# Performance work log

Measured on AMD Instinct MI355X. Metric: run time of the kernel, lower is better.

Reference implementation:

```python
import jax, jax.numpy as jnp
import numpy as np
from math import sqrt


def setup_inputs() -> dict:
    key = jax.random.key(0)
    ks = jax.random.split(key, 10)
    N, C = 192, 96  # C = N // 2
    n, h, w = 8, 64, 64
    s = lambda fan_in: 1.0 / np.sqrt(fan_in)
    return {
        "x": jax.random.normal(ks[0], (n, N, h, w), dtype=jnp.float32),
        "pe": jax.random.normal(ks[1], (N, 120, 120), dtype=jnp.float32) * 0.02,
        "wq": jax.random.normal(ks[2], (C, N), dtype=jnp.float32) * s(N),
        "bq": jax.random.normal(ks[3], (C,), dtype=jnp.float32) * 0.01,
        "wk": jax.random.normal(ks[4], (C, N), dtype=jnp.float32) * s(N),
        "bk": jax.random.normal(ks[5], (C,), dtype=jnp.float32) * 0.01,
        "wv": jax.random.normal(ks[6], (C, N), dtype=jnp.float32) * s(N),
        "bv": jax.random.normal(ks[7], (C,), dtype=jnp.float32) * 0.01,
        "wz": jax.random.normal(ks[8], (N, C), dtype=jnp.float32) * s(C),
        "bz": jax.random.normal(ks[9], (N,), dtype=jnp.float32) * 0.01,
    }


def _conv1x1(x, w, b):
    # x: [n, cin, h, w]; w: [cout, cin]; b: [cout]
    return jnp.einsum("oc,nchw->nohw", w, x) + b[None, :, None, None]


def reference(x, pe, wq, bq, wk, bk, wv, bv, wz, bz):
    n, c_in, h, w = x.shape
    hw = h * w
    # 2D positional encoding, sliced to the actual spatial size
    x = x + pe[None, :, :h, :w]
    c = wq.shape[0]  # N // 2
    q = _conv1x1(x, wq, bq).reshape(n, c, hw)   # [n, c, hw]
    k = _conv1x1(x, wk, bk).reshape(n, c, hw)   # [n, c, hw]
    v = _conv1x1(x, wv, bv).reshape(n, c, hw)   # [n, c, hw]
    scale = sqrt(hw)
    # logits[n, i, j] = sum_c q[n,c,i] * k[n,c,j]
    logits = jnp.einsum("nci,ncj->nij", q, k) / scale  # [n, hw, hw]
    weights = jax.nn.softmax(logits, axis=-1)
    # z[n, c, i] = sum_j weights[n,i,j] * v[n,c,j]
    z = jnp.einsum("nij,ncj->nci", weights, v).reshape(n, c, h, w)
    z = _conv1x1(z, wz, bz)  # [n, N, h, w]
    return x + z
```

## Files before the change

### kernel.cpp

```cpp
#include <hip/hip_runtime.h>
#include <hip/hip_bf16.h>

#define HW 4096
#define CIN 192
#define CMID 96

typedef __attribute__((ext_vector_type(8))) short bf16x8;
typedef __attribute__((ext_vector_type(4))) float f32x4;
typedef __attribute__((ext_vector_type(16))) float f32x16;
typedef __attribute__((ext_vector_type(4))) unsigned int u32x4;

static __device__ __forceinline__ unsigned short f2bf(float f) {
    union { float f; unsigned int u; } v;
    v.f = f;
    unsigned int r = v.u + 0x7fffu + ((v.u >> 16) & 1u);
    return (unsigned short)(r >> 16);
}
static __device__ __forceinline__ float b2f(unsigned short h) {
    union { unsigned int u; float f; } v;
    v.u = ((unsigned int)h) << 16;
    return v.f;
}

static __device__ __forceinline__ void gload16(const void* g, void* l) {
    __builtin_amdgcn_global_load_lds(
        (const __attribute__((address_space(1))) unsigned int*)g,
        (__attribute__((address_space(3))) unsigned int*)l, 16, 0, 0);
}

#define SCQ (0.015625f * 1.44269504089f)

__global__ __launch_bounds__(256) void convw_kernel(
    const float* __restrict__ wq, const float* __restrict__ wk,
    const float* __restrict__ wv, const float* __restrict__ wz,
    unsigned short* __restrict__ wqkvb, unsigned short* __restrict__ wzb)
{
    int idx = blockIdx.x * 256 + threadIdx.x;
    if (idx < 3 * CMID * CIN) {
        int m = idx / (CMID * CIN), r = idx % (CMID * CIN);
        const float* w = (m == 0) ? wq : ((m == 1) ? wk : wv);
        wqkvb[idx] = f2bf(w[r]);
    } else if (idx < 3 * CMID * CIN + CIN * CMID) {
        int r = idx - 3 * CMID * CIN;
        wzb[r] = f2bf(wz[r]);
    }
}

__global__ __launch_bounds__(256) void qkv_kernel(
    const float* __restrict__ x, const float* __restrict__ pe,
    const unsigned short* __restrict__ wqkvb,
    const float* __restrict__ bq, const float* __restrict__ bk,
    const float* __restrict__ bv,
    unsigned short* __restrict__ Q, unsigned short* __restrict__ K,
    unsigned short* __restrict__ V)
{
    const int n = blockIdx.y, i0 = blockIdx.x * 64, t = threadIdx.x;
    __shared__ unsigned short xt[64 * 200];

    for (int idx = t; idx < CIN * 64; idx += 256) {
        int c = idx >> 6, il = idx & 63;
        float v = x[((size_t)n * CIN + c) * HW + i0 + il]
                + pe[c * 14400 + blockIdx.x * 120 + il];
        xt[il * 200 + c] = f2bf(v);
    }
    __syncthreads();

    const int w = t >> 6, lane = t & 63, l15 = lane & 15, lg = lane >> 4;
    const int p0 = w * 16;

    bf16x8 af[6];
    #pragma unroll
    for (int f = 0; f < 6; ++f)
        af[f] = *(const bf16x8*)(xt + (p0 + l15) * 200 + f * 32 + lg * 8);

    #pragma unroll
    for (int ct = 0; ct < 18; ++ct) {
        const int m = ct / 6, c6 = ct % 6;
        f32x4 acc = (f32x4){0.f, 0.f, 0.f, 0.f};
        const unsigned short* wrow = wqkvb + (ct * 16 + l15) * CIN + lg * 8;
        #pragma unroll
        for (int f = 0; f < 6; ++f) {
            bf16x8 wf = *(const bf16x8*)(wrow + f * 32);
            if (m < 2)
                acc = __builtin_amdgcn_mfma_f32_16x16x32_bf16(wf, af[f], acc, 0, 0, 0);
            else
                acc = __builtin_amdgcn_mfma_f32_16x16x32_bf16(af[f], wf, acc, 0, 0, 0);
        }
        if (m < 2) {
            f32x4 bv4 = *(const f32x4*)(((m == 0) ? bq : bk) + c6 * 16 + lg * 4);
            ushort4 pk4;
            if (m == 0) {
                pk4.x = f2bf((acc[0] + bv4[0]) * SCQ);
                pk4.y = f2bf((acc[1] + bv4[1]) * SCQ);
                pk4.z = f2bf((acc[2] + bv4[2]) * SCQ);
                pk4.w = f2bf((acc[3] + bv4[3]) * SCQ);
            } else {
                pk4.x = f2bf(acc[0] + bv4[0]);
                pk4.y = f2bf(acc[1] + bv4[1]);
                pk4.z = f2bf(acc[2] + bv4[2]);
                pk4.w = f2bf(acc[3] + bv4[3]);
            }
            unsigned short* dst = ((m == 0) ? Q : K) + (size_t)n * HW * CMID;
            *(ushort4*)(dst + (size_t)(i0 + p0 + l15) * CMID + c6 * 16 + lg * 4) = pk4;
        } else {
            const float bias = bv[c6 * 16 + l15];
            ushort4 pk4;
            pk4.x = f2bf(acc[0] + bias); pk4.y = f2bf(acc[1] + bias);
            pk4.z = f2bf(acc[2] + bias); pk4.w = f2bf(acc[3] + bias);
            *(ushort4*)(V + (size_t)n * CMID * HW + (size_t)(c6 * 16 + l15) * HW
                          + i0 + p0 + lg * 4) = pk4;
        }
    }
}

__global__ __launch_bounds__(256, 4) void attn_kernel(
    const unsigned short* __restrict__ Q, const unsigned short* __restrict__ K,
    const unsigned short* __restrict__ V,
    unsigned short* __restrict__ zp, float* __restrict__ lp)
{
    const int bid = blockIdx.x;
    const int n  = bid & 7;
    const int jh = bid >> 8;
    const int bx = (bid >> 3) & 31;

    const int t = threadIdx.x, w = t >> 6, lane = t & 63;
    const int l31 = lane & 31, hi = lane >> 5;
    const int ib = bx * 128 + w * 32;

    __shared__ unsigned short Ks[2][32 * 128];
    __shared__ unsigned short Vs[2][96 * 64];

    const unsigned short* Qb = Q + (size_t)n * HW * CMID;
    const unsigned short* Kb = K + (size_t)n * HW * CMID;
    const unsigned short* Vb = V + (size_t)n * CMID * HW;

    bf16x8 qf[6];
    #pragma unroll
    for (int kc = 0; kc < 6; ++kc)
        qf[kc] = *(const bf16x8*)(Qb + (size_t)(ib + l31) * CMID + kc * 16 + hi * 8);

    int ksoff[2], vsoff[3];
    #pragma unroll
    for (int s = 0; s < 2; ++s) {
        int row = 4 * (w * 2 + s) + (lane >> 4);
        ksoff[s] = row * CMID + (((lane & 15) ^ (row & 7)) * 8);
    }
    #pragma unroll
    for (int s = 0; s < 3; ++s) {
        int c = 8 * (w * 3 + s) + (lane >> 3);
        vsoff[s] = c * HW + (((lane & 7) ^ (c & 7)) * 8);
    }

#define STAGE_K(J0, BUF) do {                                                      \
    _Pragma("unroll") for (int s = 0; s < 2; ++s)                                  \
        gload16(Kb + (size_t)(J0) * CMID + ksoff[s], &Ks[BUF][(w * 2 + s) * 512]); \
} while (0)
#define STAGE_V(J0, BUF) do {                                                      \
    _Pragma("unroll") for (int s = 0; s < 3; ++s)                                  \
        gload16(Vb + (size_t)(J0) + vsoff[s], &Vs[BUF][(w * 3 + s) * 512]);        \
} while (0)

    const int j00 = jh * 1024;
    STAGE_K(j00, 0);
    STAGE_V(j00, 0);

    f32x16 O[3];
    #pragma unroll
    for (int e = 0; e < 16; ++e) { O[0][e] = 0.f; O[1][e] = 0.f; O[2][e] = 0.f; }
    float lsum = 0.f;

    __syncthreads();

    for (int tt = 0; tt < 32; ++tt) {
        if (tt < 31) STAGE_K(j00 + (tt + 1) * 32, (tt + 1) & 1);
        if ((tt & 1) == 0 && tt < 30)
            STAGE_V(j00 + ((tt >> 1) + 1) * 64, ((tt >> 1) + 1) & 1);

        const unsigned short* Kc = Ks[tt & 1];
        const unsigned short* Vc = Vs[(tt >> 1) & 1];
        const int vhalf = tt & 1;

        f32x16 sacc;
        #pragma unroll
        for (int e = 0; e < 16; ++e) sacc[e] = 0.f;
        __builtin_amdgcn_s_setprio(1);
        #pragma unroll
        for (int kc = 0; kc < 6; ++kc) {
            bf16x8 kf = *(const bf16x8*)(Kc + l31 * 128
                                           + ((((kc * 2 + hi) ^ (l31 & 7))) << 3));
            sacc = __builtin_amdgcn_mfma_f32_32x32x16_bf16(kf, qf[kc], sacc, 0, 0, 0);
        }
        __builtin_amdgcn_s_setprio(0);

        unsigned pkk[4][2];
        #pragma unroll
        for (int q = 0; q < 4; ++q)
            #pragma unroll
            for (int rp = 0; rp < 2; ++rp) {
                float lo = exp2f(sacc[q * 4 + 2 * rp]);
                float hh = exp2f(sacc[q * 4 + 2 * rp + 1]);
                lsum += lo + hh;
                unsigned d;
                asm("v_cvt_pk_bf16_f32 %0, %1, %2" : "=v"(d) : "v"(lo), "v"(hh));
                pkk[q][rp] = d;
            }

        u32x4 pfu[2];
        #pragma unroll
        for (int p = 0; p < 2; ++p)
            #pragma unroll
            for (int rp = 0; rp < 2; ++rp) {
                unsigned A = pkk[2 * p][rp], B = pkk[2 * p + 1][rp];
                unsigned Ax = (unsigned)__shfl_xor((int)A, 32, 64);
                unsigned Bx = (unsigned)__shfl_xor((int)B, 32, 64);
                pfu[p][rp]     = hi ? Bx : A;
                pfu[p][2 + rp] = hi ? B  : Ax;
            }

        __builtin_amdgcn_s_setprio(1);
        #pragma unroll
        for (int jc = 0; jc < 2; ++jc) {
            bf16x8 pfv = __builtin_bit_cast(bf16x8, pfu[jc]);
            #pragma unroll
            for (int cc = 0; cc < 3; ++cc) {
                bf16x8 vf = *(const bf16x8*)(Vc + (cc * 32 + l31) * 64
                    + ((((vhalf * 4 + jc * 2 + hi) ^ (l31 & 7))) << 3));
                O[cc] = __builtin_amdgcn_mfma_f32_32x32x16_bf16(pfv, vf, O[cc], 0, 0, 0);
            }
        }
        __builtin_amdgcn_s_setprio(0);

        __syncthreads();
    }
#undef STAGE_K
#undef STAGE_V

    unsigned short* zb = zp + ((size_t)jh * 8 + n) * HW * CMID;
    #pragma unroll
    for (int cc = 0; cc < 3; ++cc)
        #pragma unroll
        for (int r = 0; r < 16; ++r) {
            int i = (r & 3) + 8 * (r >> 2) + 4 * hi;
            zb[(size_t)(ib + i) * CMID + cc * 32 + l31] = f2bf(O[cc][r]);
        }

    lsum += __shfl_xor(lsum, 32, 64);
    if (hi == 0) {
        float* lb = lp + ((size_t)jh * 8 + n) * HW;
        lb[ib + l31] = lsum;
    }
}

__global__ __launch_bounds__(256) void zproj_kernel(
    const unsigned short* __restrict__ zp, const float* __restrict__ lp,
    const unsigned short* __restrict__ wzb, const float* __restrict__ bz,
    const float* __restrict__ x, const float* __restrict__ pe,
    float* __restrict__ out)
{
    const int n = blockIdx.y, i0 = blockIdx.x * 64, t = threadIdx.x;
    __shared__ unsigned short zt[64 * 104];
    __shared__ float ll[64];

    if (t < 64) {
        float s = 0.f;
        #pragma unroll
        for (int sl = 0; sl < 4; ++sl)
            s += lp[(size_t)sl * 8 * HW + (size_t)n * HW + i0 + t];
        ll[t] = 1.f / s;
    }
    __syncthreads();

    for (int idx = t; idx < 64 * 24; idx += 256) {
        int i = idx / 24, c4 = (idx % 24) * 4;
        size_t gidx = ((size_t)n * HW + i0 + i) * CMID + c4;
        float a0 = 0.f, a1 = 0.f, a2 = 0.f, a3 = 0.f;
        #pragma unroll
        for (int sl = 0; sl < 4; ++sl) {
            ushort4 a = *(const ushort4*)(zp + (size_t)sl * 8 * HW * CMID + gidx);
            a0 += b2f(a.x); a1 += b2f(a.y); a2 += b2f(a.z); a3 += b2f(a.w);
        }
        float li = ll[i];
        zt[i * 104 + c4 + 0] = f2bf(a0 * li);
        zt[i * 104 + c4 + 1] = f2bf(a1 * li);
        zt[i * 104 + c4 + 2] = f2bf(a2 * li);
        zt[i * 104 + c4 + 3] = f2bf(a3 * li);
    }
    __syncthreads();

    const int w = t >> 6, lane = t & 63, l15 = lane & 15, lg = lane >> 4;
    const int p0 = w * 16;

    bf16x8 af[3];
    #pragma unroll
    for (int f = 0; f < 3; ++f)
        af[f] = *(const bf16x8*)(zt + (p0 + l15) * 104 + f * 32 + lg * 8);

    #pragma unroll
    for (int ct = 0; ct < 12; ++ct) {
        f32x4 acc = (f32x4){0.f, 0.f, 0.f, 0.f};
        const unsigned short* wrow = wzb + (ct * 16 + l15) * CMID + lg * 8;
        #pragma unroll
        for (int f = 0; f < 3; ++f) {
            bf16x8 wf = *(const bf16x8*)(wrow + f * 32);
            acc = __builtin_amdgcn_mfma_f32_16x16x32_bf16(af[f], wf, acc, 0, 0, 0);
        }
        const int co = ct * 16 + l15;
        const int ibase = i0 + p0 + lg * 4;
        size_t xa = ((size_t)n * CIN + co) * HW + ibase;
        f32x4 xv = *(const f32x4*)(x + xa);
        f32x4 pv = *(const f32x4*)(pe + co * 14400 + blockIdx.x * 120 + p0 + lg * 4);
        const float bias = bz[co];
        f32x4 o;
        #pragma unroll
        for (int r = 0; r < 4; ++r) o[r] = xv[r] + pv[r] + acc[r] + bias;
        *(f32x4*)(out + xa) = o;
    }
}

extern "C" void kernel_launch(void* const* d_in, const int* in_sizes, int n_in,
                              void* d_out, int out_size, void* d_ws, size_t ws_size,
                              hipStream_t stream) {
    const float* x  = (const float*)d_in[0];
    const float* pe = (const float*)d_in[1];
    const float* wq = (const float*)d_in[2];
    const float* bq = (const float*)d_in[3];
    const float* wk = (const float*)d_in[4];
    const float* bk = (const float*)d_in[5];
    const float* wv = (const float*)d_in[6];
    const float* bv = (const float*)d_in[7];
    const float* wz = (const float*)d_in[8];
    const float* bz = (const float*)d_in[9];
    float* out = (float*)d_out;

    char* ws = (char*)d_ws;
    unsigned short* wqkvb = (unsigned short*)(ws);
    unsigned short* wzb   = (unsigned short*)(ws + 131072);
    unsigned short* Qb    = (unsigned short*)(ws + 196608);
    unsigned short* Kb    = (unsigned short*)(ws + 6488064);
    unsigned short* Vb    = (unsigned short*)(ws + 12779520);
    unsigned short* zpb   = (unsigned short*)(ws + 19070976);
    float*          lpb   = (float*)(ws + 44236800);

    convw_kernel<<<288, 256, 0, stream>>>(wq, wk, wv, wz, wqkvb, wzb);
    qkv_kernel<<<dim3(64, 8), 256, 0, stream>>>(x, pe, wqkvb, bq, bk, bv,
                                                Qb, Kb, Vb);
    attn_kernel<<<1024, 256, 0, stream>>>(Qb, Kb, Vb, zpb, lpb);
    zproj_kernel<<<dim3(64, 8), 256, 0, stream>>>(zpb, lpb, wzb, bz, x, pe, out);
}
```

Measured before the change: 130.2 us.

## Process two query sub-tiles per wave with triple-buffered K staging

Each wave now handles 64 query rows (two 32-row sub-tiles) instead of 32, so every K and V fragment read from shared memory feeds two MFMAs. The grid is halved to 512 blocks. K staging moves to a triple-buffered ring with explicit vmcnt waits and raw barriers, and the lane-half shuffle is replaced by v_permlane32_swap. In exchange, register pressure roughly doubles (launch bounds drop to 2 blocks per SM) and there are fewer blocks to spread across the CUs.

Measured after the change: 124.6 us. 1.04x faster.

```diff
diff --git a/kernel.cpp b/kernel.cpp
--- a/kernel.cpp
+++ b/kernel.cpp
@@ -113,36 +113,39 @@
     }
 }
 
-__global__ __launch_bounds__(256, 4) void attn_kernel(
+__global__ __launch_bounds__(256, 2) void attn_kernel(
     const unsigned short* __restrict__ Q, const unsigned short* __restrict__ K,
     const unsigned short* __restrict__ V,
     unsigned short* __restrict__ zp, float* __restrict__ lp)
 {
     const int bid = blockIdx.x;
-    const int n  = bid & 7;
-    const int jh = bid >> 8;
-    const int bx = (bid >> 3) & 31;
+    const int n    = bid & 7;
+    const int iblk = (bid >> 3) & 15;
+    const int js   = bid >> 7;
 
     const int t = threadIdx.x, w = t >> 6, lane = t & 63;
     const int l31 = lane & 31, hi = lane >> 5;
-    const int ib = bx * 128 + w * 32;
-
-    __shared__ unsigned short Ks[2][32 * 128];
+    const int ib = iblk * 256 + w * 64;
+
+    __shared__ unsigned short Ks[3][32 * 128];
     __shared__ unsigned short Vs[2][96 * 64];
 
     const unsigned short* Qb = Q + (size_t)n * HW * CMID;
     const unsigned short* Kb = K + (size_t)n * HW * CMID;
     const unsigned short* Vb = V + (size_t)n * CMID * HW;
 
-    bf16x8 qf[6];
-    #pragma unroll
-    for (int kc = 0; kc < 6; ++kc)
-        qf[kc] = *(const bf16x8*)(Qb + (size_t)(ib + l31) * CMID + kc * 16 + hi * 8);
+    bf16x8 qf[2][6];
+    #pragma unroll
+    for (int is = 0; is < 2; ++is)
+        #pragma unroll
+        for (int kc = 0; kc < 6; ++kc)
+            qf[is][kc] = *(const bf16x8*)(Qb + (size_t)(ib + is * 32 + l31) * CMID
+                                            + kc * 16 + hi * 8);
 
     int ksoff[2], vsoff[3];
     #pragma unroll
     for (int s = 0; s < 2; ++s) {
-        int row = 4 * (w * 2 + s) + (lane >> 4);
+        int row = 8 * w + 4 * s + (lane >> 4);
         ksoff[s] = row * CMID + (((lane & 15) ^ (row & 7)) * 8);
     }
     #pragma unroll
@@ -151,103 +154,129 @@
         vsoff[s] = c * HW + (((lane & 7) ^ (c & 7)) * 8);
     }
 
-#define STAGE_K(J0, BUF) do {                                                      \
-    _Pragma("unroll") for (int s = 0; s < 2; ++s)                                  \
-        gload16(Kb + (size_t)(J0) * CMID + ksoff[s], &Ks[BUF][(w * 2 + s) * 512]); \
+    const int j00 = js * 1024;
+
+#define STAGE_K(TILE, KB) do {                                                 \
+    _Pragma("unroll") for (int s = 0; s < 2; ++s)                              \
+        gload16(Kb + (size_t)(j00 + (TILE) * 32) * CMID + ksoff[s],            \
+                &Ks[KB][(w * 2 + s) * 512]);                                   \
 } while (0)
-#define STAGE_V(J0, BUF) do {                                                      \
-    _Pragma("unroll") for (int s = 0; s < 3; ++s)                                  \
-        gload16(Vb + (size_t)(J0) + vsoff[s], &Vs[BUF][(w * 3 + s) * 512]);        \
+#define STAGE_V(WND, VB) do {                                                  \
+    _Pragma("unroll") for (int s = 0; s < 3; ++s)                              \
+        gload16(Vb + (size_t)(j00 + (WND) * 64) + vsoff[s],                    \
+                &Vs[VB][(w * 3 + s) * 512]);                                   \
 } while (0)
 
-    const int j00 = jh * 1024;
-    STAGE_K(j00, 0);
-    STAGE_V(j00, 0);
-
-    f32x16 O[3];
-    #pragma unroll
-    for (int e = 0; e < 16; ++e) { O[0][e] = 0.f; O[1][e] = 0.f; O[2][e] = 0.f; }
-    float lsum = 0.f;
-
-    __syncthreads();
-
-    for (int tt = 0; tt < 32; ++tt) {
-        if (tt < 31) STAGE_K(j00 + (tt + 1) * 32, (tt + 1) & 1);
-        if ((tt & 1) == 0 && tt < 30)
-            STAGE_V(j00 + ((tt >> 1) + 1) * 64, ((tt >> 1) + 1) & 1);
-
-        const unsigned short* Kc = Ks[tt & 1];
-        const unsigned short* Vc = Vs[(tt >> 1) & 1];
-        const int vhalf = tt & 1;
-
-        f32x16 sacc;
-        #pragma unroll
-        for (int e = 0; e < 16; ++e) sacc[e] = 0.f;
-        __builtin_amdgcn_s_setprio(1);
-        #pragma unroll
-        for (int kc = 0; kc < 6; ++kc) {
-            bf16x8 kf = *(const bf16x8*)(Kc + l31 * 128
-                                           + ((((kc * 2 + hi) ^ (l31 & 7))) << 3));
-            sacc = __builtin_amdgcn_mfma_f32_32x32x16_bf16(kf, qf[kc], sacc, 0, 0, 0);
-        }
-        __builtin_amdgcn_s_setprio(0);
-
-        unsigned pkk[4][2];
-        #pragma unroll
-        for (int q = 0; q < 4; ++q)
+    f32x16 O[2][3];
+    #pragma unroll
+    for (int is = 0; is < 2; ++is)
+        #pragma unroll
+        for (int cc = 0; cc < 3; ++cc)
             #pragma unroll
-            for (int rp = 0; rp < 2; ++rp) {
-                float lo = exp2f(sacc[q * 4 + 2 * rp]);
-                float hh = exp2f(sacc[q * 4 + 2 * rp + 1]);
-                lsum += lo + hh;
-                unsigned d;
-                asm("v_cvt_pk_bf16_f32 %0, %1, %2" : "=v"(d) : "v"(lo), "v"(hh));
-                pkk[q][rp] = d;
-            }
-
-        u32x4 pfu[2];
-        #pragma unroll
-        for (int p = 0; p < 2; ++p)
-            #pragma unroll
-            for (int rp = 0; rp < 2; ++rp) {
-                unsigned A = pkk[2 * p][rp], B = pkk[2 * p + 1][rp];
-                unsigned Ax = (unsigned)__shfl_xor((int)A, 32, 64);
-                unsigned Bx = (unsigned)__shfl_xor((int)B, 32, 64);
-                pfu[p][rp]     = hi ? Bx : A;
-                pfu[p][2 + rp] = hi ? B  : Ax;
-            }
-
-        __builtin_amdgcn_s_setprio(1);
-        #pragma unroll
-        for (int jc = 0; jc < 2; ++jc) {
-            bf16x8 pfv = __builtin_bit_cast(bf16x8, pfu[jc]);
-            #pragma unroll
-            for (int cc = 0; cc < 3; ++cc) {
-                bf16x8 vf = *(const bf16x8*)(Vc + (cc * 32 + l31) * 64
-                    + ((((vhalf * 4 + jc * 2 + hi) ^ (l31 & 7))) << 3));
-                O[cc] = __builtin_amdgcn_mfma_f32_32x32x16_bf16(pfv, vf, O[cc], 0, 0, 0);
-            }
-        }
-        __builtin_amdgcn_s_setprio(0);
-
-        __syncthreads();
-    }
+            for (int e = 0; e < 16; ++e) O[is][cc][e] = 0.f;
+    float lsum0 = 0.f, lsum1 = 0.f;
+
+    STAGE_K(0, 0);
+    STAGE_K(1, 1);
+    STAGE_V(0, 0);
+    asm volatile("s_waitcnt vmcnt(0)" ::: "memory");
+    __builtin_amdgcn_s_barrier();
+
+#define BODY(KBUF, VBUF, VHALF) do {                                           \
+    const unsigned short* Kc = &Ks[KBUF][0];                                   \
+    const unsigned short* Vc = &Vs[VBUF][0];                                   \
+    f32x16 s0, s1;                                                             \
+    _Pragma("unroll") for (int e = 0; e < 16; ++e) { s0[e] = 0.f; s1[e] = 0.f; } \
+    __builtin_amdgcn_s_setprio(1);                                             \
+    _Pragma("unroll") for (int kc = 0; kc < 6; ++kc) {                         \
+        bf16x8 kf = *(const bf16x8*)(Kc + l31 * 128 +                          \
+                      (((kc * 2 + hi) ^ (l31 & 7)) << 3));                     \
+        s0 = __builtin_amdgcn_mfma_f32_32x32x16_bf16(kf, qf[0][kc], s0, 0, 0, 0); \
+        s1 = __builtin_amdgcn_mfma_f32_32x32x16_bf16(kf, qf[1][kc], s1, 0, 0, 0); \
+    }                                                                          \
+    __builtin_amdgcn_s_setprio(0);                                             \
+    unsigned pkk[2][4][2];                                                     \
+    _Pragma("unroll") for (int q = 0; q < 4; ++q)                              \
+        _Pragma("unroll") for (int rp = 0; rp < 2; ++rp) {                     \
+            float lo0 = __builtin_exp2f(s0[q * 4 + 2 * rp]);                   \
+            float hh0 = __builtin_exp2f(s0[q * 4 + 2 * rp + 1]);               \
+            float lo1 = __builtin_exp2f(s1[q * 4 + 2 * rp]);                   \
+            float hh1 = __builtin_exp2f(s1[q * 4 + 2 * rp + 1]);               \
+            lsum0 += lo0 + hh0; lsum1 += lo1 + hh1;                            \
+            asm("v_cvt_pk_bf16_f32 %0, %1, %2"                                 \
+                : "=v"(pkk[0][q][rp]) : "v"(lo0), "v"(hh0));                   \
+            asm("v_cvt_pk_bf16_f32 %0, %1, %2"                                 \
+                : "=v"(pkk[1][q][rp]) : "v"(lo1), "v"(hh1));                   \
+        }                                                                      \
+    u32x4 pfu[2][2];                                                           \
+    _Pragma("unroll") for (int is = 0; is < 2; ++is)                           \
+        _Pragma("unroll") for (int jc = 0; jc < 2; ++jc) {                     \
+            unsigned x0 = pkk[is][2 * jc][0], y0 = pkk[is][2 * jc + 1][0];     \
+            unsigned x1 = pkk[is][2 * jc][1], y1 = pkk[is][2 * jc + 1][1];     \
+            asm("v_permlane32_swap_b32 %0, %1" : "+v"(y0), "+v"(x0));          \
+            asm("v_permlane32_swap_b32 %0, %1" : "+v"(y1), "+v"(x1));          \
+            pfu[is][jc][0] = x0; pfu[is][jc][1] = x1;                          \
+            pfu[is][jc][2] = y0; pfu[is][jc][3] = y1;                          \
+        }                                                                      \
+    __builtin_amdgcn_s_setprio(1);                                             \
+    _Pragma("unroll") for (int jc = 0; jc < 2; ++jc) {                         \
+        bf16x8 pa0 = __builtin_bit_cast(bf16x8, pfu[0][jc]);                   \
+        bf16x8 pa1 = __builtin_bit_cast(bf16x8, pfu[1][jc]);                   \
+        _Pragma("unroll") for (int cc = 0; cc < 3; ++cc) {                     \
+            bf16x8 vf = *(const bf16x8*)(Vc + (cc * 32 + l31) * 64 +           \
+                          ((((VHALF) * 4 + jc * 2 + hi) ^ (l31 & 7)) << 3));   \
+            O[0][cc] = __builtin_amdgcn_mfma_f32_32x32x16_bf16(pa0, vf, O[0][cc], 0, 0, 0); \
+            O[1][cc] = __builtin_amdgcn_mfma_f32_32x32x16_bf16(pa1, vf, O[1][cc], 0, 0, 0); \
+        }                                                                      \
+    }                                                                          \
+    __builtin_amdgcn_s_setprio(0);                                             \
+} while (0)
+
+    int kb = 0, kb1 = 1, kb2 = 2;
+    for (int tt = 0; tt < 32; tt += 2) {
+        {
+            const int pfk = (tt + 2 < 32) ? tt + 2 : 31;
+            STAGE_K(pfk, kb2);
+            const int wn = (tt >> 1) + 1;
+            const int pfw = (wn < 16) ? wn : 15;
+            STAGE_V(pfw, wn & 1);
+            BODY(kb, (tt >> 1) & 1, 0);
+            asm volatile("s_waitcnt vmcnt(5)" ::: "memory");
+            __builtin_amdgcn_s_barrier();
+        }
+        {
+            const int pfk = (tt + 3 < 32) ? tt + 3 : 31;
+            STAGE_K(pfk, kb);
+            BODY(kb1, (tt >> 1) & 1, 1);
+            asm volatile("s_waitcnt vmcnt(2)" ::: "memory");
+            __builtin_amdgcn_s_barrier();
+        }
+        const int tmp = kb;
+        kb = kb2; kb2 = kb1; kb1 = tmp;
+    }
+#undef BODY
 #undef STAGE_K
 #undef STAGE_V
 
-    unsigned short* zb = zp + ((size_t)jh * 8 + n) * HW * CMID;
-    #pragma unroll
-    for (int cc = 0; cc < 3; ++cc)
-        #pragma unroll
-        for (int r = 0; r < 16; ++r) {
-            int i = (r & 3) + 8 * (r >> 2) + 4 * hi;
-            zb[(size_t)(ib + i) * CMID + cc * 32 + l31] = f2bf(O[cc][r]);
-        }
-
-    lsum += __shfl_xor(lsum, 32, 64);
+    asm volatile("s_waitcnt vmcnt(0)" ::: "memory");
+
+    unsigned short* zb = zp + ((size_t)js * 8 + n) * HW * CMID;
+    #pragma unroll
+    for (int is = 0; is < 2; ++is)
+        #pragma unroll
+        for (int cc = 0; cc < 3; ++cc)
+            #pragma unroll
+            for (int r = 0; r < 16; ++r) {
+                int i = ib + is * 32 + (r & 3) + 8 * (r >> 2) + 4 * hi;
+                zb[(size_t)i * CMID + cc * 32 + l31] = f2bf(O[is][cc][r]);
+            }
+
+    lsum0 += __shfl_xor(lsum0, 32, 64);
+    lsum1 += __shfl_xor(lsum1, 32, 64);
     if (hi == 0) {
-        float* lb = lp + ((size_t)jh * 8 + n) * HW;
-        lb[ib + l31] = lsum;
+        float* lb = lp + ((size_t)js * 8 + n) * HW;
+        lb[ib + l31]      = lsum0;
+        lb[ib + 32 + l31] = lsum1;
     }
 }
 
@@ -344,6 +373,6 @@
     convw_kernel<<<288, 256, 0, stream>>>(wq, wk, wv, wz, wqkvb, wzb);
     qkv_kernel<<<dim3(64, 8), 256, 0, stream>>>(x, pe, wqkvb, bq, bk, bv,
                                                 Qb, Kb, Vb);
-    attn_kernel<<<1024, 256, 0, stream>>>(Qb, Kb, Vb, zpb, lpb);
+    attn_kernel<<<512, 256, 0, stream>>>(Qb, Kb, Vb, zpb, lpb);
     zproj_kernel<<<dim3(64, 8), 256, 0, stream>>>(zpb, lpb, wzb, bz, x, pe, out);
 }
```
